# Kernel tuning notes

Measured on AMD Instinct MI355X. Metric: run time of the kernel, lower is better.

The kernel has to match this reference:

```python
import jax, jax.numpy as jnp
import numpy as np

ATTN_HEAD = 8
ATTN_EMB = 16


def setup_inputs() -> dict:
    key = jax.random.key(0)
    ks = jax.random.split(key, 5)
    B, F, D = 1024, 128, 128
    return {
        "inputs": jax.random.normal(ks[0], (B, F, D), dtype=jnp.float32),
        "W_query": jax.random.normal(ks[1], (D, ATTN_HEAD * ATTN_EMB), dtype=jnp.float32) * 0.05,
        "W_key": jax.random.normal(ks[2], (D, ATTN_HEAD * ATTN_EMB), dtype=jnp.float32) * 0.05,
        "W_value": jax.random.normal(ks[3], (D, ATTN_HEAD * ATTN_EMB), dtype=jnp.float32) * 0.05,
        "W_res": jax.random.normal(ks[4], (D, ATTN_HEAD * ATTN_EMB), dtype=jnp.float32) * 0.05,
    }


def _proj_heads(x, W, H, d):
    # [B,F,D] @ [D,H*d] -> [B,H,F,d]; tf.split+stack(axis=1) == reshape+transpose
    B, F, _ = x.shape
    y = jnp.einsum('bfd,de->bfe', x, W)
    return y.reshape(B, F, H, d).transpose(0, 2, 1, 3)


def reference(inputs, W_query, W_key, W_value, W_res):
    B, F, D = inputs.shape
    H, d = ATTN_HEAD, ATTN_EMB
    Q = _proj_heads(inputs, W_query, H, d)
    K = _proj_heads(inputs, W_key, H, d)
    V = _proj_heads(inputs, W_value, H, d)
    # NOTE: original scales by sqrt(feat_dim), not sqrt(head_dim)
    scale = 1.0 / (float(D) ** 0.5)
    scores = jnp.einsum('bhqd,bhkd->bhqk', Q, K) * scale
    attn = jax.nn.softmax(scores, axis=-1)
    out = jnp.einsum('bhqk,bhkd->bhqd', attn, V)
    out = out + _proj_heads(inputs, W_res, H, d)
    # [B,H,F,d] -> [B,F,H,d] -> [B,F,D]
    return out.transpose(0, 2, 1, 3).reshape(B, F, D)
```

## Files before the change

### kernel.cpp

```cpp
#include <hip/hip_runtime.h>
#include <hip/hip_bf16.h>
#include <stdint.h>


typedef __attribute__((ext_vector_type(8))) short short8;
typedef __attribute__((ext_vector_type(16))) float f32x16;
typedef __attribute__((ext_vector_type(4))) unsigned int uint4v;
typedef __attribute__((ext_vector_type(2))) unsigned int uint2v;
typedef unsigned short ushort_t;
typedef unsigned int uint_t;

#define KF_OFF 0
#define QF_OFF 8192
#define VT_OFF 16384
#define ONES_OFF 24576

__device__ __forceinline__ ushort_t b16(float f) {
  return __builtin_bit_cast(ushort_t, __float2bfloat16(f));
}
__device__ __forceinline__ uint_t rnd(float f) {
  return __float_as_uint(f) + 0x8000u;
}
__device__ __forceinline__ uint_t pk2(float a, float b) {
  return __byte_perm(rnd(a), rnd(b), 0x7632);
}
__device__ __forceinline__ uint_t pk2t(float a, float b) {
  return __byte_perm(__float_as_uint(a), __float_as_uint(b), 0x7632);
}
__device__ __forceinline__ ushort_t b16d(float f) {
  return (ushort_t)(rnd(f) >> 16);
}

__global__ void prep_w(const float* __restrict__ Wq, const float* __restrict__ Wk,
                       const float* __restrict__ Wv, const float* __restrict__ Wr,
                       ushort_t* __restrict__ wt) {
  int i = blockIdx.x * 256 + threadIdx.x;
  int u = i >> 9;
  int l = (i >> 3) & 63;
  int j = i & 7;
  int p = u >> 5, np = (u >> 3) & 3, kk = u & 7;
  int col = 32 * np + (l & 31);
  int d = kk * 16 + ((l >> 5) & 1) * 8 + j;
  const float* W = (p == 0) ? Wq : (p == 1) ? Wk : (p == 2) ? Wv : Wr;
  float scl = (p == 0) ? 0.12751459f : 1.0f;
  wt[i] = b16(W[d * 128 + col] * scl);
}

__global__ __launch_bounds__(256, 3) void mha21(const float* __restrict__ X,
                                                const ushort_t* __restrict__ wt,
                                                float* __restrict__ out) {
  __shared__ char lds[24832];
  const int t = threadIdx.x;
  const int w = t >> 6, l = t & 63;
  const int i = blockIdx.x;
  const int b = (i & 7) * 128 + (i >> 5);
  const int hq = (i >> 3) & 3;
  const int hi5 = l >> 5, q = l & 31, e = l & 15, hb = (l >> 4) & 1;

  if (t < 16) {
    uint4v ones = {0x3F803F80u, 0x3F803F80u, 0x3F803F80u, 0x3F803F80u};
    *(uint4v*)(lds + ONES_OFF + t * 16) = ones;
  }

  const float* xrow = X + (((size_t)b * 128) + 32 * w + q) * 128;
  short8 afr[8];
#pragma unroll
  for (int kk = 0; kk < 8; ++kk) {
    float4 a = *(const float4*)(xrow + kk * 16 + 8 * hi5);
    float4 c4 = *(const float4*)(xrow + kk * 16 + 8 * hi5 + 4);
    uint4v u = {pk2(a.x, a.y), pk2(a.z, a.w), pk2(c4.x, c4.y), pk2(c4.z, c4.w)};
    afr[kk] = __builtin_bit_cast(short8, u);
  }

  const short8* wf = (const short8*)wt;
  auto proj = [&](int p) {
    f32x16 acc = {};
#pragma unroll
    for (int kk = 0; kk < 8; ++kk) {
      short8 bfr = wf[((p * 4 + hq) * 8 + kk) * 64 + l];
      acc = __builtin_amdgcn_mfma_f32_32x32x16_bf16(afr[kk], bfr, acc, 0, 0, 0);
    }
    return acc;
  };
  auto st_qk = [&](int off, const f32x16& d) {
    const int uxor = ((e >> 3) | (hb << 1));
    char* p = lds + off + hb * 4096 + w * 1024 + 512 * (e >> 3) +
              (e & 7) * 2 + 64 * hi5;
#pragma unroll
    for (int r = 0; r < 16; ++r) {
      int u = (r & 3) + 8 * (r >> 2);
      *(ushort_t*)(p + 16 * (u ^ uxor)) = b16d(d[r]);
    }
  };
  auto st_v = [&](const f32x16& d) {
#pragma unroll
    for (int q2 = 0; q2 < 4; ++q2) {
      int f0 = 32 * w + 8 * q2 + 4 * hi5;
      uint2v pk = {pk2(d[4 * q2 + 0], d[4 * q2 + 1]),
                   pk2(d[4 * q2 + 2], d[4 * q2 + 3])};
      *(uint2v*)(lds + VT_OFF + hb * 4096 + e * 256 +
                 ((f0 * 2) ^ ((e & 7) << 4))) = pk;
    }
  };

  f32x16 Ra;
  {
    f32x16 d;
    d = proj(0); st_qk(QF_OFF, d);
    d = proj(1); st_qk(KF_OFF, d);
    d = proj(2); st_v(d);
    Ra = proj(3);
  }
  __syncthreads();

  const int sw0 = hi5 << 4;
  const int sw1 = (hi5 | 2) << 4;
  short8 qf0 = *(const short8*)(lds + QF_OFF + w * 1024 + ((l * 16) ^ sw0));
  short8 qf1 = *(const short8*)(lds + QF_OFF + 4096 + w * 1024 +
                                ((l * 16) ^ sw1));
  const char* vb0 = (q == 16) ? (lds + ONES_OFF) : (lds + VT_OFF);
  const char* vb1 = (q == 0) ? (lds + ONES_OFF) : (lds + VT_OFF + 4096);

  f32x16 oA = {}, oB = {};
  auto finish = [&](f32x16& s, f32x16& o, const char* vb, int tt) {
#pragma unroll
    for (int r = 0; r < 16; ++r) s[r] = __builtin_amdgcn_exp2f(s[r]);
#pragma unroll
    for (int gg = 0; gg < 2; ++gg) {
      int rb = gg * 8, g = 2 * tt + gg;
      uint_t wl  = pk2t(s[rb + 0], s[rb + 1]);
      uint_t wl2 = pk2t(s[rb + 2], s[rb + 3]);
      uint_t wh  = pk2t(s[rb + 4], s[rb + 5]);
      uint_t wh2 = pk2t(s[rb + 6], s[rb + 7]);
      uint2v r0 = __builtin_amdgcn_permlane32_swap(wl, wh, false, false);
      uint2v r1 = __builtin_amdgcn_permlane32_swap(wl2, wh2, false, false);
      uint4v pw = {r0[0], r1[0], r0[1], r1[1]};
      short8 pa = __builtin_bit_cast(short8, pw);
      short8 vfr = *(const short8*)(vb + e * 256 +
                                    ((32 * g + 16 * hi5) ^ ((e & 7) << 4)));
      __builtin_amdgcn_s_setprio(1);
      o = __builtin_amdgcn_mfma_f32_32x32x16_bf16(pa, vfr, o, 0, 0, 0);
      __builtin_amdgcn_s_setprio(0);
    }
  };

#pragma unroll
  for (int tt = 0; tt < 4; ++tt) {
    short8 kf0 = *(const short8*)(lds + KF_OFF + tt * 1024 + ((l * 16) ^ sw0));
    short8 kf1 = *(const short8*)(lds + KF_OFF + 4096 + tt * 1024 +
                                  ((l * 16) ^ sw1));
    f32x16 z0 = {}, z1 = {};
    __builtin_amdgcn_s_setprio(1);
    f32x16 s0 = __builtin_amdgcn_mfma_f32_32x32x16_bf16(kf0, qf0, z0, 0, 0, 0);
    f32x16 s1 = __builtin_amdgcn_mfma_f32_32x32x16_bf16(kf1, qf1, z1, 0, 0, 0);
    __builtin_amdgcn_s_setprio(0);
    finish(s0, oA, vb0, tt);
    finish(s1, oB, vb1, tt);
  }

  const int srcl = (l & 32) | (hb ? 0 : 16);
#pragma unroll
  for (int r = 0; r < 16; ++r) {
    int row = (r & 3) + 8 * (r >> 2) + 4 * hi5;
    float d = (q == 16) ? oA[r] : oB[r];
    float s = __shfl(d, srcl, 64);
    float rsr = __builtin_amdgcn_rcpf(s);
    float ov = hb ? oB[r] : oA[r];
    float val = __builtin_fmaf(ov, rsr, Ra[r]);
    out[(((size_t)b * 128) + 32 * w + row) * 128 + 32 * hq + q] = val;
  }
}

extern "C" void kernel_launch(void* const* d_in, const int* in_sizes, int n_in,
                              void* d_out, int out_size, void* d_ws, size_t ws_size,
                              hipStream_t stream) {
  const float* X  = (const float*)d_in[0];
  const float* Wq = (const float*)d_in[1];
  const float* Wk = (const float*)d_in[2];
  const float* Wv = (const float*)d_in[3];
  const float* Wr = (const float*)d_in[4];
  float* out = (float*)d_out;
  ushort_t* wt = (ushort_t*)d_ws;

  hipLaunchKernelGGL(prep_w, dim3(256), dim3(256), 0, stream, Wq, Wk, Wv, Wr, wt);
  hipLaunchKernelGGL(mha21, dim3(4096), dim3(256), 0, stream, X, wt, out);
}
```

Before: 62.53 us.

## Process head halves sequentially and spill residual projection to LDS as bf16

The attention phase now handles the two head halves one after the other instead of interleaving them, so only one output accumulator is live at a time. The residual projection is packed to bf16 and parked in LDS (36-byte per-thread stride) instead of sitting in registers, and the explicit launch_bounds is dropped. The goal is lower register pressure and possibly higher occupancy. In exchange it loses ILP between the two interleaved MFMA chains, grows LDS per block, and rounds the residual term to bf16, which lowers precision.

Measured after the change: 72.04 us. 15.2% more time.

```diff
diff --git a/kernel.cpp b/kernel.cpp
--- a/kernel.cpp
+++ b/kernel.cpp
@@ -14,6 +14,8 @@
 #define QF_OFF 8192
 #define VT_OFF 16384
 #define ONES_OFF 24576
+#define RA_OFF 24832
+#define LDS_SZ 34048
 
 __device__ __forceinline__ ushort_t b16(float f) {
   return __builtin_bit_cast(ushort_t, __float2bfloat16(f));
@@ -46,10 +48,10 @@
   wt[i] = b16(W[d * 128 + col] * scl);
 }
 
-__global__ __launch_bounds__(256, 3) void mha21(const float* __restrict__ X,
-                                                const ushort_t* __restrict__ wt,
-                                                float* __restrict__ out) {
-  __shared__ char lds[24832];
+__global__ void mha22(const float* __restrict__ X,
+                      const ushort_t* __restrict__ wt,
+                      float* __restrict__ out) {
+  __shared__ char lds[LDS_SZ];
   const int t = threadIdx.x;
   const int w = t >> 6, l = t & 63;
   const int i = blockIdx.x;
@@ -103,71 +105,71 @@
     }
   };
 
-  f32x16 Ra;
   {
     f32x16 d;
     d = proj(0); st_qk(QF_OFF, d);
     d = proj(1); st_qk(KF_OFF, d);
     d = proj(2); st_v(d);
-    Ra = proj(3);
+    d = proj(3);
+#pragma unroll
+    for (int r2 = 0; r2 < 8; ++r2)
+      *(uint_t*)(lds + RA_OFF + t * 36 + r2 * 4) = pk2(d[2 * r2], d[2 * r2 + 1]);
   }
   __syncthreads();
 
-  const int sw0 = hi5 << 4;
-  const int sw1 = (hi5 | 2) << 4;
-  short8 qf0 = *(const short8*)(lds + QF_OFF + w * 1024 + ((l * 16) ^ sw0));
-  short8 qf1 = *(const short8*)(lds + QF_OFF + 4096 + w * 1024 +
-                                ((l * 16) ^ sw1));
-  const char* vb0 = (q == 16) ? (lds + ONES_OFF) : (lds + VT_OFF);
-  const char* vb1 = (q == 0) ? (lds + ONES_OFF) : (lds + VT_OFF + 4096);
-
-  f32x16 oA = {}, oB = {};
-  auto finish = [&](f32x16& s, f32x16& o, const char* vb, int tt) {
 #pragma unroll
-    for (int r = 0; r < 16; ++r) s[r] = __builtin_amdgcn_exp2f(s[r]);
+  for (int h = 0; h < 2; ++h) {
+    const int sw = (hi5 | (h << 1)) << 4;
+    short8 qf = *(const short8*)(lds + QF_OFF + h * 4096 + w * 1024 +
+                                 ((l * 16) ^ sw));
+    const char* vb = (h == 0)
+        ? ((q == 16) ? (lds + ONES_OFF) : (lds + VT_OFF))
+        : ((q == 0) ? (lds + ONES_OFF) : (lds + VT_OFF + 4096));
+    f32x16 o = {};
 #pragma unroll
-    for (int gg = 0; gg < 2; ++gg) {
-      int rb = gg * 8, g = 2 * tt + gg;
-      uint_t wl  = pk2t(s[rb + 0], s[rb + 1]);
-      uint_t wl2 = pk2t(s[rb + 2], s[rb + 3]);
-      uint_t wh  = pk2t(s[rb + 4], s[rb + 5]);
-      uint_t wh2 = pk2t(s[rb + 6], s[rb + 7]);
-      uint2v r0 = __builtin_amdgcn_permlane32_swap(wl, wh, false, false);
-      uint2v r1 = __builtin_amdgcn_permlane32_swap(wl2, wh2, false, false);
-      uint4v pw = {r0[0], r1[0], r0[1], r1[1]};
-      short8 pa = __builtin_bit_cast(short8, pw);
-      short8 vfr = *(const short8*)(vb + e * 256 +
-                                    ((32 * g + 16 * hi5) ^ ((e & 7) << 4)));
+    for (int tt = 0; tt < 4; ++tt) {
+      short8 kf = *(const short8*)(lds + KF_OFF + h * 4096 + tt * 1024 +
+                                   ((l * 16) ^ sw));
+      f32x16 z = {};
       __builtin_amdgcn_s_setprio(1);
-      o = __builtin_amdgcn_mfma_f32_32x32x16_bf16(pa, vfr, o, 0, 0, 0);
+      f32x16 s = __builtin_amdgcn_mfma_f32_32x32x16_bf16(kf, qf, z, 0, 0, 0);
       __builtin_amdgcn_s_setprio(0);
+#pragma unroll
+      for (int r = 0; r < 16; ++r) s[r] = __builtin_amdgcn_exp2f(s[r]);
+#pragma unroll
+      for (int gg = 0; gg < 2; ++gg) {
+        int rb = gg * 8, g = 2 * tt + gg;
+        uint_t wl  = pk2t(s[rb + 0], s[rb + 1]);
+        uint_t wl2 = pk2t(s[rb + 2], s[rb + 3]);
+        uint_t wh  = pk2t(s[rb + 4], s[rb + 5]);
+        uint_t wh2 = pk2t(s[rb + 6], s[rb + 7]);
+        uint2v r0 = __builtin_amdgcn_permlane32_swap(wl, wh, false, false);
+        uint2v r1 = __builtin_amdgcn_permlane32_swap(wl2, wh2, false, false);
+        uint4v pw = {r0[0], r1[0], r0[1], r1[1]};
+        short8 pa = __builtin_bit_cast(short8, pw);
+        short8 vfr = *(const short8*)(vb + e * 256 +
+                                      ((32 * g + 16 * hi5) ^ ((e & 7) << 4)));
+        __builtin_amdgcn_s_setprio(1);
+        o = __builtin_amdgcn_mfma_f32_32x32x16_bf16(pa, vfr, o, 0, 0, 0);
+        __builtin_amdgcn_s_setprio(0);
+      }
     }
-  };
-
+    const int srcl = (l & 32) | (h ? 0 : 16);
 #pragma unroll
-  for (int tt = 0; tt < 4; ++tt) {
-    short8 kf0 = *(const short8*)(lds + KF_OFF + tt * 1024 + ((l * 16) ^ sw0));
-    short8 kf1 = *(const short8*)(lds + KF_OFF + 4096 + tt * 1024 +
-                                  ((l * 16) ^ sw1));
-    f32x16 z0 = {}, z1 = {};
-    __builtin_amdgcn_s_setprio(1);
-    f32x16 s0 = __builtin_amdgcn_mfma_f32_32x32x16_bf16(kf0, qf0, z0, 0, 0, 0);
-    f32x16 s1 = __builtin_amdgcn_mfma_f32_32x32x16_bf16(kf1, qf1, z1, 0, 0, 0);
-    __builtin_amdgcn_s_setprio(0);
-    finish(s0, oA, vb0, tt);
-    finish(s1, oB, vb1, tt);
-  }
-
-  const int srcl = (l & 32) | (hb ? 0 : 16);
+    for (int r2 = 0; r2 < 8; ++r2) {
+      uint_t rap = *(const uint_t*)(lds + RA_OFF + t * 36 + r2 * 4);
 #pragma unroll
-  for (int r = 0; r < 16; ++r) {
-    int row = (r & 3) + 8 * (r >> 2) + 4 * hi5;
-    float d = (q == 16) ? oA[r] : oB[r];
-    float s = __shfl(d, srcl, 64);
-    float rsr = __builtin_amdgcn_rcpf(s);
-    float ov = hb ? oB[r] : oA[r];
-    float val = __builtin_fmaf(ov, rsr, Ra[r]);
-    out[(((size_t)b * 128) + 32 * w + row) * 128 + 32 * hq + q] = val;
+      for (int j = 0; j < 2; ++j) {
+        int r = 2 * r2 + j;
+        float sv = __shfl(o[r], srcl, 64);
+        float rsr = __builtin_amdgcn_rcpf(sv);
+        float ra = __uint_as_float(j ? (rap & 0xffff0000u) : (rap << 16));
+        float val = __builtin_fmaf(o[r], rsr, ra);
+        int row = (r & 3) + 8 * (r >> 2) + 4 * hi5;
+        if (hb == h)
+          out[(((size_t)b * 128) + 32 * w + row) * 128 + 32 * hq + q] = val;
+      }
+    }
   }
 }
 
@@ -183,5 +185,5 @@
   ushort_t* wt = (ushort_t*)d_ws;
 
   hipLaunchKernelGGL(prep_w, dim3(256), dim3(256), 0, stream, Wq, Wk, Wv, Wr, wt);
-  hipLaunchKernelGGL(mha21, dim3(4096), dim3(256), 0, stream, X, wt, out);
+  hipLaunchKernelGGL(mha22, dim3(4096), dim3(256), 0, stream, X, wt, out);
 }
```
